# Kernel tuning notes

Hardware: AMD Instinct MI355X
Metric: run time of the kernel (lower is better)

The kernel has to match this reference:

```python
import jax, jax.numpy as jnp
import numpy as np

N_NODES = 10000
N_EDGES = 320000
IN_FEATS = 512
N_UNITS = 256
OUT_FEATS = 64
N_LAYERS = 6  # number of hidden GCNConv layers feeding the JK max


def setup_inputs() -> dict:
    key = jax.random.key(0)
    ks = jax.random.split(key, 8)
    h = jax.random.normal(ks[0], (N_NODES, IN_FEATS), dtype=jnp.float32)
    edge_index = jax.random.randint(ks[1], (2, N_EDGES), 0, N_NODES, dtype=jnp.int64)
    # learned parameters (glorot-ish scale)
    W0 = jax.random.normal(ks[2], (IN_FEATS, N_UNITS), dtype=jnp.float32) * (1.0 / np.sqrt(IN_FEATS))
    b0 = jnp.zeros((N_UNITS,), dtype=jnp.float32)
    Wh = jax.random.normal(ks[3], (N_LAYERS - 1, N_UNITS, N_UNITS), dtype=jnp.float32) * (1.0 / np.sqrt(N_UNITS))
    bh = jnp.zeros((N_LAYERS - 1, N_UNITS), dtype=jnp.float32)
    Wo = jax.random.normal(ks[4], (N_UNITS, OUT_FEATS), dtype=jnp.float32) * (1.0 / np.sqrt(N_UNITS))
    bo = jnp.zeros((OUT_FEATS,), dtype=jnp.float32)
    return {"h": h, "edge_index": edge_index, "W0": W0, "b0": b0,
            "Wh": Wh, "bh": bh, "Wo": Wo, "bo": bo}


def reference(h, edge_index, W0, b0, Wh, bh, Wo, bo):
    src = edge_index[0]
    dst = edge_index[1]
    n = h.shape[0]

    def conv_plain(x, W, b):
        # GCNConv with normalize=False: plain sum aggregation over edges, no self-loops
        m = x @ W                                   # [N, d]
        agg = jax.ops.segment_sum(m[src], dst, num_segments=n)
        return jax.nn.relu(agg + b)

    outs = []
    x = conv_plain(h, W0, b0)
    outs.append(x)
    for i in range(Wh.shape[0]):  # dropout is identity in eval mode
        x = conv_plain(x, Wh[i], bh[i])
        outs.append(x)

    # jumping-knowledge max aggregation over layer outputs
    x = jnp.max(jnp.stack(outs, axis=0), axis=0)    # [N, n_units]

    # final GCNConv with normalize=True (symmetric GCN norm, self-loops added)
    m = x @ Wo                                      # [N, out_feats]
    ones = jnp.ones(dst.shape, dtype=m.dtype)
    deg = jax.ops.segment_sum(ones, dst, num_segments=n) + 1.0  # +1 self loop
    dinv = deg ** -0.5
    coef = dinv[src] * dinv[dst]                    # [E]
    agg = jax.ops.segment_sum(m[src] * coef[:, None], dst, num_segments=n)
    agg = agg + m / deg[:, None] + bo               # self-loop term 1/deg_i
    return jax.nn.log_softmax(agg, axis=-1)
```

## Files before the change

### kernel.cpp

```cpp
#include <hip/hip_runtime.h>
#include <math.h>

#define N_NODES 10000
#define N_EDGES 320000
#define IN_FEATS 512
#define N_UNITS 256
#define OUT_FEATS 64
#define N_HID 5

typedef __attribute__((ext_vector_type(8))) short bf16x8;
typedef __attribute__((ext_vector_type(4))) float f32x4;

__device__ __forceinline__ unsigned short f2bf(float f) {
    union { float f; unsigned int u; } c; c.f = f;
    unsigned int u = c.u + 0x7FFFu + ((c.u >> 16) & 1u);
    return (unsigned short)(u >> 16);
}
__device__ __forceinline__ float bf2f(unsigned int b) {
    union { unsigned int u; float f; } c; c.u = (b & 0xffffu) << 16;
    return c.f;
}


__global__ void k_setup(const int* __restrict__ dst, int* __restrict__ deg,
                        const float* __restrict__ h, unsigned short* __restrict__ hb,
                        const float* __restrict__ W0, const float* __restrict__ Wh,
                        const float* __restrict__ Wo,
                        unsigned short* __restrict__ W0t, unsigned short* __restrict__ Wht,
                        unsigned short* __restrict__ Wot) {
    const int R1 = N_EDGES;
    const int R2 = N_NODES * IN_FEATS / 4;
    const int S0 = IN_FEATS * N_UNITS;
    const int SH = N_HID * N_UNITS * N_UNITS;
    const int SO = N_UNITS * OUT_FEATS;
    int t = blockIdx.x * blockDim.x + threadIdx.x;
    if (t < R1) {
        atomicAdd(&deg[dst[t]], 1);
    } else if (t < R1 + R2) {
        int u = t - R1;
        float4 v = reinterpret_cast<const float4*>(h)[u];
        ushort4 o;
        o.x = f2bf(v.x); o.y = f2bf(v.y); o.z = f2bf(v.z); o.w = f2bf(v.w);
        reinterpret_cast<ushort4*>(hb)[u] = o;
    } else {
        int u = t - R1 - R2;
        if (u < S0) {
            int k = u >> 8, n = u & 255;
            W0t[(size_t)n * IN_FEATS + k] = f2bf(W0[u]);
        } else if (u < S0 + SH) {
            int w = u - S0;
            int l = w >> 16, r = w & 65535;
            int k = r >> 8, n = r & 255;
            Wht[(size_t)l * 65536 + (size_t)n * N_UNITS + k] = f2bf(Wh[w]);
        } else if (u < S0 + SH + SO) {
            int w = u - S0 - SH;
            int k = w >> 6, n = w & 63;
            Wot[(size_t)n * N_UNITS + k] = f2bf(Wo[w]);
        }
    }
}


__global__ __launch_bounds__(1024) void k_scan(const int* __restrict__ deg,
                                               int* __restrict__ row_ptr,
                                               int* __restrict__ cursor,
                                               float* __restrict__ dinv,
                                               float* __restrict__ invdeg) {
    __shared__ int wsum[16];
    const int PER = 10;
    int t = threadIdx.x;
    int lane = t & 63, wid = t >> 6;
    int base = t * PER;

    int v[PER];
    int s = 0;
#pragma unroll
    for (int j = 0; j < PER; ++j) {
        int i = base + j;
        int d = (i < N_NODES) ? deg[i] : 0;
        v[j] = s;
        s += d;
    }
    int inc = s;
#pragma unroll
    for (int off = 1; off < 64; off <<= 1) {
        int y = __shfl_up(inc, off);
        if (lane >= off) inc += y;
    }
    if (lane == 63) wsum[wid] = inc;
    __syncthreads();
    if (wid == 0) {
        int w = (lane < 16) ? wsum[lane] : 0;
#pragma unroll
        for (int off = 1; off < 16; off <<= 1) {
            int y = __shfl_up(w, off);
            if (lane >= off) w += y;
        }
        if (lane < 16) wsum[lane] = w;
    }
    __syncthreads();
    int wave_excl = (wid == 0) ? 0 : wsum[wid - 1];
    int thread_excl = wave_excl + (inc - s);

#pragma unroll
    for (int j = 0; j < PER; ++j) {
        int i = base + j;
        if (i < N_NODES) {
            int rp = thread_excl + v[j];
            row_ptr[i] = rp;
            cursor[i]  = rp;
            int d = ((j + 1 < PER) ? v[j + 1] : s) - v[j];
            float dd = (float)(d + 1);
            dinv[i]   = rsqrtf(dd);
            invdeg[i] = 1.0f / dd;
        }
    }
    if (t == 1023) row_ptr[N_NODES] = thread_excl + s;
}

__global__ void k_fill(const int* __restrict__ src, const int* __restrict__ dst,
                       int* __restrict__ cursor, int* __restrict__ csr_src) {
    int e = blockIdx.x * blockDim.x + threadIdx.x;
    if (e < N_EDGES) {
        int p = atomicAdd(&cursor[dst[e]], 1);
        csr_src[p] = src[e];
    }
}


__global__ __launch_bounds__(256) void k_mgemm(const unsigned short* __restrict__ A,
                                               const unsigned short* __restrict__ Bt,
                                               unsigned short* __restrict__ C,
                                               const int M, const int K, const int Nld) {
    constexpr int BM = 64, BN = 64, BK = 32;
    __shared__ unsigned short As[2][BM * BK];
    __shared__ unsigned short Bs[2][BN * BK];

    const int tid  = threadIdx.x;
    const int wid  = tid >> 6;
    const int lane = tid & 63;
    const int wr   = wid >> 1;
    const int wc   = wid & 1;
    const int brow = blockIdx.y * BM;
    const int bcol = blockIdx.x * BN;

    const int lr = lane & 15;
    const int lk = lane >> 4;

    const int row  = tid >> 2;
    const int slot = tid & 3;
    const int sslot = slot ^ ((row >> 1) & 3);

    int gra = brow + row; if (gra >= M) gra = M - 1;
    const unsigned short* gpa = A + (size_t)gra * K + sslot * 8;
    const unsigned short* gpb = Bt + (size_t)(bcol + row) * K + sslot * 8;

    f32x4 acc[2][2];
#pragma unroll
    for (int m = 0; m < 2; ++m)
#pragma unroll
        for (int n = 0; n < 2; ++n)
            acc[m][n] = (f32x4){0.f, 0.f, 0.f, 0.f};

#define STAGE(buf, k0)                                                                      \
    do {                                                                                    \
        __builtin_amdgcn_global_load_lds(                                                   \
            (const __attribute__((address_space(1))) void*)(gpa + (k0)),                    \
            (__attribute__((address_space(3))) void*)(&As[(buf)][tid * 8]), 16, 0, 0);      \
        __builtin_amdgcn_global_load_lds(                                                   \
            (const __attribute__((address_space(1))) void*)(gpb + (k0)),                    \
            (__attribute__((address_space(3))) void*)(&Bs[(buf)][tid * 8]), 16, 0, 0);      \
    } while (0)

    STAGE(0, 0);
    __syncthreads();

    const int nk = K / BK;
    for (int kt = 0; kt < nk; ++kt) {
        const int cur = kt & 1;
        if (kt + 1 < nk) STAGE(cur ^ 1, (kt + 1) * BK);

        bf16x8 af[2], bfr[2];
#pragma unroll
        for (int m = 0; m < 2; ++m) {
            int ra = wr * 32 + m * 16 + lr;
            af[m] = *reinterpret_cast<const bf16x8*>(&As[cur][ra * BK + (lk ^ ((ra >> 1) & 3)) * 8]);
        }
#pragma unroll
        for (int n = 0; n < 2; ++n) {
            int rb = wc * 32 + n * 16 + lr;
            bfr[n] = *reinterpret_cast<const bf16x8*>(&Bs[cur][rb * BK + (lk ^ ((rb >> 1) & 3)) * 8]);
        }
#pragma unroll
        for (int m = 0; m < 2; ++m)
#pragma unroll
            for (int n = 0; n < 2; ++n)
                acc[m][n] = __builtin_amdgcn_mfma_f32_16x16x32_bf16(af[m], bfr[n], acc[m][n], 0, 0, 0);
        __syncthreads();
    }
#undef STAGE

#pragma unroll
    for (int m = 0; m < 2; ++m) {
#pragma unroll
        for (int r = 0; r < 4; ++r) {
            int orow = brow + wr * 32 + m * 16 + lk * 4 + r;
            if (orow < M) {
#pragma unroll
                for (int n = 0; n < 2; ++n) {
                    int ocol = bcol + wc * 32 + n * 16 + lr;
                    C[(size_t)orow * Nld + ocol] = f2bf(acc[m][n][r]);
                }
            }
        }
    }
}


__global__ __launch_bounds__(256) void k_wgemm(const unsigned short* __restrict__ A,
                                               const unsigned short* __restrict__ Bt,
                                               unsigned short* __restrict__ C,
                                               const int M, const int Nld) {
    constexpr int K = 256;
    __shared__ unsigned short As[64 * K];
    __shared__ unsigned short Bs[64 * K];

    const int tid  = threadIdx.x;
    const int wid  = tid >> 6;
    const int lane = tid & 63;
    const int lr   = lane & 15;
    const int lk   = lane >> 4;
    const int brow = blockIdx.y * 64;
    const int bcol = blockIdx.x * 64;

#pragma unroll
    for (int p = 0; p < 8; ++p) {
        int i = p * 256 + tid;
        int row = i >> 5, s = i & 31;
        int gr = brow + row; if (gr >= M) gr = M - 1;
        const unsigned short* gp = A + (size_t)gr * K + ((s ^ (row & 7)) * 8);
        __builtin_amdgcn_global_load_lds(
            (const __attribute__((address_space(1))) void*)gp,
            (__attribute__((address_space(3))) void*)(As + i * 8), 16, 0, 0);
    }
#pragma unroll
    for (int p = 0; p < 8; ++p) {
        int i = p * 256 + tid;
        int row = i >> 5, s = i & 31;
        const unsigned short* gp = Bt + (size_t)(bcol + row) * K + ((s ^ (row & 7)) * 8);
        __builtin_amdgcn_global_load_lds(
            (const __attribute__((address_space(1))) void*)gp,
            (__attribute__((address_space(3))) void*)(Bs + i * 8), 16, 0, 0);
    }
    __syncthreads();

    f32x4 acc[4];
#pragma unroll
    for (int n = 0; n < 4; ++n) acc[n] = (f32x4){0.f, 0.f, 0.f, 0.f};

    const int ra = (wid << 4) + lr;
    const unsigned short* Arow = As + ra * K;
    const int e = lr & 7;
#pragma unroll
    for (int kk = 0; kk < 8; ++kk) {
        bf16x8 av = *reinterpret_cast<const bf16x8*>(&Arow[(((kk << 2) + lk) ^ e) * 8]);
#pragma unroll
        for (int n = 0; n < 4; ++n) {
            const unsigned short* Brow = Bs + ((n << 4) + lr) * K;
            bf16x8 bv = *reinterpret_cast<const bf16x8*>(&Brow[(((kk << 2) + lk) ^ e) * 8]);
            acc[n] = __builtin_amdgcn_mfma_f32_16x16x32_bf16(av, bv, acc[n], 0, 0, 0);
        }
    }

#pragma unroll
    for (int n = 0; n < 4; ++n) {
#pragma unroll
        for (int r = 0; r < 4; ++r) {
            int orow = brow + (wid << 4) + (lk << 2) + r;
            if (orow < M) {
                int ocol = bcol + (n << 4) + lr;
                C[(size_t)orow * Nld + ocol] = f2bf(acc[n][r]);
            }
        }
    }
}


__global__ __launch_bounds__(256) void k_agg(const unsigned short* __restrict__ m,
                                             const int* __restrict__ row_ptr,
                                             const int* __restrict__ csr_src,
                                             const float* __restrict__ bias,
                                             unsigned short* __restrict__ x_out,
                                             unsigned short* __restrict__ jk,
                                             int init_jk) {
    int half = threadIdx.x >> 5;
    int lane = threadIdx.x & 31;
    int n = blockIdx.x * 8 + half;
    int s = row_ptr[n], e = row_ptr[n + 1];
    const uint4* mv = (const uint4*)m;

    float a[8];
#pragma unroll
    for (int j = 0; j < 8; ++j) a[j] = 0.f;

#define ACC8(u)                                        \
    do {                                               \
        a[0] += bf2f((u).x); a[1] += bf2f((u).x >> 16);\
        a[2] += bf2f((u).y); a[3] += bf2f((u).y >> 16);\
        a[4] += bf2f((u).z); a[5] += bf2f((u).z >> 16);\
        a[6] += bf2f((u).w); a[7] += bf2f((u).w >> 16);\
    } while (0)

    int i = s;
    for (; i + 7 < e; i += 8) {
        int idx[8];
#pragma unroll
        for (int q = 0; q < 8; ++q) idx[q] = csr_src[i + q];
        uint4 u[8];
#pragma unroll
        for (int q = 0; q < 8; ++q) u[q] = mv[(size_t)idx[q] * 32 + lane];
#pragma unroll
        for (int q = 0; q < 8; ++q) ACC8(u[q]);
    }
    for (; i < e; ++i) {
        uint4 u = mv[(size_t)csr_src[i] * 32 + lane];
        ACC8(u);
    }
#undef ACC8

    float4 b0 = ((const float4*)bias)[lane * 2];
    float4 b1 = ((const float4*)bias)[lane * 2 + 1];
    unsigned int hh[8];
    hh[0] = f2bf(fmaxf(a[0] + b0.x, 0.f));
    hh[1] = f2bf(fmaxf(a[1] + b0.y, 0.f));
    hh[2] = f2bf(fmaxf(a[2] + b0.z, 0.f));
    hh[3] = f2bf(fmaxf(a[3] + b0.w, 0.f));
    hh[4] = f2bf(fmaxf(a[4] + b1.x, 0.f));
    hh[5] = f2bf(fmaxf(a[5] + b1.y, 0.f));
    hh[6] = f2bf(fmaxf(a[6] + b1.z, 0.f));
    hh[7] = f2bf(fmaxf(a[7] + b1.w, 0.f));
    uint4 o;
    o.x = hh[0] | (hh[1] << 16);
    o.y = hh[2] | (hh[3] << 16);
    o.z = hh[4] | (hh[5] << 16);
    o.w = hh[6] | (hh[7] << 16);

    size_t idx = (size_t)n * 32 + lane;
    ((uint4*)x_out)[idx] = o;
    if (init_jk) {
        ((uint4*)jk)[idx] = o;
    } else {
        uint4 j = ((const uint4*)jk)[idx];
        auto mx2 = [](unsigned int nw, unsigned int od) {
            unsigned int lo_n = nw & 0xffffu, lo_o = od & 0xffffu;
            unsigned int hi_n = nw >> 16,     hi_o = od >> 16;
            unsigned int lo = lo_n > lo_o ? lo_n : lo_o;
            unsigned int hi = hi_n > hi_o ? hi_n : hi_o;
            return lo | (hi << 16);
        };
        uint4 w;
        w.x = mx2(o.x, j.x); w.y = mx2(o.y, j.y);
        w.z = mx2(o.z, j.z); w.w = mx2(o.w, j.w);
        ((uint4*)jk)[idx] = w;
    }
}


__global__ __launch_bounds__(256) void k_final(const unsigned short* __restrict__ mf,
                                               const int* __restrict__ row_ptr,
                                               const int* __restrict__ csr_src,
                                               const float* __restrict__ dinv,
                                               const float* __restrict__ invdeg,
                                               const float* __restrict__ bo,
                                               float* __restrict__ out) {
    int halfw = threadIdx.x >> 5;
    int wl = threadIdx.x & 31;
    const unsigned int* mfu = (const unsigned int*)mf;
    int n = blockIdx.x * 8 + halfw;
    int s = row_ptr[n], e = row_ptr[n + 1];

    float a0 = 0.f, a1 = 0.f;
    int i = s;
    for (; i + 3 < e; i += 4) {
        int i0 = csr_src[i], i1 = csr_src[i + 1], i2 = csr_src[i + 2], i3 = csr_src[i + 3];
        unsigned int u0 = mfu[(size_t)i0 * 32 + wl];
        unsigned int u1 = mfu[(size_t)i1 * 32 + wl];
        unsigned int u2 = mfu[(size_t)i2 * 32 + wl];
        unsigned int u3 = mfu[(size_t)i3 * 32 + wl];
        float d0 = dinv[i0], d1 = dinv[i1], d2 = dinv[i2], d3 = dinv[i3];
        a0 += bf2f(u0) * d0 + bf2f(u1) * d1 + bf2f(u2) * d2 + bf2f(u3) * d3;
        a1 += bf2f(u0 >> 16) * d0 + bf2f(u1 >> 16) * d1 + bf2f(u2 >> 16) * d2 + bf2f(u3 >> 16) * d3;
    }
    for (; i < e; ++i) {
        int sr = csr_src[i];
        unsigned int u = mfu[(size_t)sr * 32 + wl];
        float dv = dinv[sr];
        a0 += bf2f(u) * dv;
        a1 += bf2f(u >> 16) * dv;
    }
    float dn = dinv[n];
    a0 *= dn; a1 *= dn;
    unsigned int un = mfu[(size_t)n * 32 + wl];
    float idg = invdeg[n];
    float2 bo2 = ((const float2*)bo)[wl];
    a0 += bf2f(un) * idg + bo2.x;
    a1 += bf2f(un >> 16) * idg + bo2.y;

    float mx = fmaxf(a0, a1);
#pragma unroll
    for (int off = 16; off; off >>= 1) mx = fmaxf(mx, __shfl_xor(mx, off));
    float e0 = __expf(a0 - mx), e1 = __expf(a1 - mx);
    float sum = e0 + e1;
#pragma unroll
    for (int off = 16; off; off >>= 1) sum += __shfl_xor(sum, off);
    float ls = __logf(sum);
    float2 r;
    r.x = a0 - mx - ls;
    r.y = a1 - mx - ls;
    ((float2*)out)[(size_t)n * 32 + wl] = r;
}


extern "C" void kernel_launch(void* const* d_in, const int* in_sizes, int n_in,
                              void* d_out, int out_size, void* d_ws, size_t ws_size,
                              hipStream_t stream) {
    const float* h  = (const float*)d_in[0];
    const int*   ei = (const int*)d_in[1];
    const float* W0 = (const float*)d_in[2];
    const float* b0 = (const float*)d_in[3];
    const float* Wh = (const float*)d_in[4];
    const float* bh = (const float*)d_in[5];
    const float* Wo = (const float*)d_in[6];
    const float* bo = (const float*)d_in[7];

    const int* src = ei;
    const int* dst = ei + N_EDGES;

    char* p = (char*)d_ws;
    auto carve = [&](size_t bytes) {
        char* r = p;
        p += (bytes + 255) & ~(size_t)255;
        return r;
    };
    int*   deg     = (int*)  carve(N_NODES * 4);
    int*   row_ptr = (int*)  carve((N_NODES + 1) * 4);
    int*   cursor  = (int*)  carve(N_NODES * 4);
    int*   csr_src = (int*)  carve(N_EDGES * 4);
    float* dinv    = (float*)carve(N_NODES * 4);
    float* invdeg  = (float*)carve(N_NODES * 4);
    unsigned short* hb  = (unsigned short*)carve((size_t)N_NODES * IN_FEATS * 2);
    unsigned short* W0t = (unsigned short*)carve((size_t)IN_FEATS * N_UNITS * 2);
    unsigned short* Wht = (unsigned short*)carve((size_t)N_HID * N_UNITS * N_UNITS * 2);
    unsigned short* Wot = (unsigned short*)carve((size_t)N_UNITS * OUT_FEATS * 2);
    unsigned short* m   = (unsigned short*)carve((size_t)N_NODES * N_UNITS * 2);
    unsigned short* x   = (unsigned short*)carve((size_t)N_NODES * N_UNITS * 2);
    unsigned short* jk  = (unsigned short*)carve((size_t)N_NODES * N_UNITS * 2);
    unsigned short* mf  = (unsigned short*)carve((size_t)N_NODES * OUT_FEATS * 2);

    hipMemsetAsync(deg, 0, N_NODES * 4, stream);
    {
        const int total = N_EDGES + N_NODES * IN_FEATS / 4 +
                          IN_FEATS * N_UNITS + N_HID * N_UNITS * N_UNITS + N_UNITS * OUT_FEATS;
        k_setup<<<(total + 255) / 256, 256, 0, stream>>>(dst, deg, h, hb, W0, Wh, Wo,
                                                         W0t, Wht, Wot);
    }
    k_scan<<<1, 1024, 0, stream>>>(deg, row_ptr, cursor, dinv, invdeg);
    k_fill<<<(N_EDGES + 255) / 256, 256, 0, stream>>>(src, dst, cursor, csr_src);

    const int GBM = (N_NODES + 63) / 64;

    {
        dim3 g(N_UNITS / 64, GBM);
        k_mgemm<<<g, 256, 0, stream>>>(hb, W0t, m, N_NODES, IN_FEATS, N_UNITS);
    }
    k_agg<<<N_NODES / 8, 256, 0, stream>>>(m, row_ptr, csr_src, b0, x, jk, 1);

    for (int l = 0; l < N_HID; ++l) {
        dim3 g(N_UNITS / 64, GBM);
        k_wgemm<<<g, 256, 0, stream>>>(x, Wht + (size_t)l * N_UNITS * N_UNITS, m,
                                       N_NODES, N_UNITS);
        k_agg<<<N_NODES / 8, 256, 0, stream>>>(m, row_ptr, csr_src, bh + (size_t)l * N_UNITS,
                                               x, jk, 0);
    }

    {
        dim3 g(1, GBM);
        k_wgemm<<<g, 256, 0, stream>>>(jk, Wot, mf, N_NODES, OUT_FEATS);
    }
    k_final<<<N_NODES / 8, 256, 0, stream>>>(mf, row_ptr, csr_src, dinv, invdeg,
                                             bo, (float*)d_out);
}
```

Before: 253.3 us.

## Fuse fp32-to-bf16 input conversion into first GEMM and skip final x write

Removes the separate pass that converts the fp32 input features to bf16 in the setup kernel. The first-layer GEMM now loads fp32 rows directly, converts them in registers and stores bf16 into shared memory, using a full-width 256-column tile so each A row is read once. The last hidden aggregation layer also skips writing x, since only the JK max buffer is used afterwards. The trade-off is that the A loads become synchronous register loads instead of async global-to-LDS copies, and the larger tile means fewer blocks and more accumulator registers.

After: 256.6 us. About the same (+1.3%).

```diff
diff --git a/kernel.cpp b/kernel.cpp
--- a/kernel.cpp
+++ b/kernel.cpp
@@ -23,27 +23,19 @@
 
 
 __global__ void k_setup(const int* __restrict__ dst, int* __restrict__ deg,
-                        const float* __restrict__ h, unsigned short* __restrict__ hb,
                         const float* __restrict__ W0, const float* __restrict__ Wh,
                         const float* __restrict__ Wo,
                         unsigned short* __restrict__ W0t, unsigned short* __restrict__ Wht,
                         unsigned short* __restrict__ Wot) {
     const int R1 = N_EDGES;
-    const int R2 = N_NODES * IN_FEATS / 4;
     const int S0 = IN_FEATS * N_UNITS;
     const int SH = N_HID * N_UNITS * N_UNITS;
     const int SO = N_UNITS * OUT_FEATS;
     int t = blockIdx.x * blockDim.x + threadIdx.x;
     if (t < R1) {
         atomicAdd(&deg[dst[t]], 1);
-    } else if (t < R1 + R2) {
+    } else {
         int u = t - R1;
-        float4 v = reinterpret_cast<const float4*>(h)[u];
-        ushort4 o;
-        o.x = f2bf(v.x); o.y = f2bf(v.y); o.z = f2bf(v.z); o.w = f2bf(v.w);
-        reinterpret_cast<ushort4*>(hb)[u] = o;
-    } else {
-        int u = t - R1 - R2;
         if (u < S0) {
             int k = u >> 8, n = u & 255;
             W0t[(size_t)n * IN_FEATS + k] = f2bf(W0[u]);
@@ -128,88 +120,107 @@
 }
 
 
-__global__ __launch_bounds__(256) void k_mgemm(const unsigned short* __restrict__ A,
-                                               const unsigned short* __restrict__ Bt,
-                                               unsigned short* __restrict__ C,
-                                               const int M, const int K, const int Nld) {
-    constexpr int BM = 64, BN = 64, BK = 32;
-    __shared__ unsigned short As[2][BM * BK];
-    __shared__ unsigned short Bs[2][BN * BK];
+__global__ __launch_bounds__(256) void k_mgemm_h(const float* __restrict__ h,
+                                                 const unsigned short* __restrict__ Bt,
+                                                 unsigned short* __restrict__ C) {
+    constexpr int K = IN_FEATS;
+    constexpr int BM = 64, BN = 256, BK = 32;
+    __shared__ unsigned short As[2 * BM * BK];
+    __shared__ unsigned short Bs[2 * BN * BK];
 
     const int tid  = threadIdx.x;
     const int wid  = tid >> 6;
     const int lane = tid & 63;
     const int wr   = wid >> 1;
     const int wc   = wid & 1;
-    const int brow = blockIdx.y * BM;
-    const int bcol = blockIdx.x * BN;
+    const int brow = blockIdx.x * BM;
 
     const int lr = lane & 15;
     const int lk = lane >> 4;
 
-    const int row  = tid >> 2;
-    const int slot = tid & 3;
-    const int sslot = slot ^ ((row >> 1) & 3);
-
-    int gra = brow + row; if (gra >= M) gra = M - 1;
-    const unsigned short* gpa = A + (size_t)gra * K + sslot * 8;
-    const unsigned short* gpb = Bt + (size_t)(bcol + row) * K + sslot * 8;
-
-    f32x4 acc[2][2];
+    const int arow = tid >> 2;
+    const int aseg = tid & 3;
+    const int asl  = aseg ^ ((arow >> 1) & 3);
+    int gra = brow + arow; if (gra >= N_NODES) gra = N_NODES - 1;
+    const float* ap = h + (size_t)gra * K + aseg * 8;
+
+    f32x4 acc[2][8];
 #pragma unroll
     for (int m = 0; m < 2; ++m)
 #pragma unroll
-        for (int n = 0; n < 2; ++n)
+        for (int n = 0; n < 8; ++n)
             acc[m][n] = (f32x4){0.f, 0.f, 0.f, 0.f};
 
-#define STAGE(buf, k0)                                                                      \
-    do {                                                                                    \
-        __builtin_amdgcn_global_load_lds(                                                   \
-            (const __attribute__((address_space(1))) void*)(gpa + (k0)),                    \
-            (__attribute__((address_space(3))) void*)(&As[(buf)][tid * 8]), 16, 0, 0);      \
-        __builtin_amdgcn_global_load_lds(                                                   \
-            (const __attribute__((address_space(1))) void*)(gpb + (k0)),                    \
-            (__attribute__((address_space(3))) void*)(&Bs[(buf)][tid * 8]), 16, 0, 0);      \
+#define STAGE_A(buf, k0)                                                        \
+    do {                                                                        \
+        float4 v0 = *reinterpret_cast<const float4*>(ap + (k0));                \
+        float4 v1 = *reinterpret_cast<const float4*>(ap + (k0) + 4);            \
+        uint4 o;                                                                \
+        o.x = f2bf(v0.x) | ((unsigned)f2bf(v0.y) << 16);                        \
+        o.y = f2bf(v0.z) | ((unsigned)f2bf(v0.w) << 16);                        \
+        o.z = f2bf(v1.x) | ((unsigned)f2bf(v1.y) << 16);                        \
+        o.w = f2bf(v1.z) | ((unsigned)f2bf(v1.w) << 16);                        \
+        ((uint4*)As)[(buf) * 256 + arow * 4 + asl] = o;                         \
     } while (0)
 
-    STAGE(0, 0);
+#define STAGE_B(buf, k0)                                                                     \
+    do {                                                                                     \
+        _Pragma("unroll")                                                                    \
+        for (int p = 0; p < 4; ++p) {                                                        \
+            int i2 = p * 256 + tid;                                                          \
+            int row = i2 >> 2, sx = i2 & 3;                                                  \
+            const unsigned short* gp =                                                       \
+                Bt + (size_t)row * K + (k0) + ((sx ^ ((row >> 1) & 3)) * 8);                 \
+            __builtin_amdgcn_global_load_lds(                                                \
+                (const __attribute__((address_space(1))) void*)gp,                           \
+                (__attribute__((address_space(3))) void*)(Bs + (buf) * BN * BK + i2 * 8),    \
+                16, 0, 0);                                                                   \
+        }                                                                                    \
+    } while (0)
+
+    STAGE_A(0, 0);
+    STAGE_B(0, 0);
     __syncthreads();
 
     const int nk = K / BK;
     for (int kt = 0; kt < nk; ++kt) {
         const int cur = kt & 1;
-        if (kt + 1 < nk) STAGE(cur ^ 1, (kt + 1) * BK);
-
-        bf16x8 af[2], bfr[2];
+        if (kt + 1 < nk) {
+            STAGE_A(cur ^ 1, (kt + 1) * BK);
+            STAGE_B(cur ^ 1, (kt + 1) * BK);
+        }
+
+        bf16x8 af[2], bfr[8];
 #pragma unroll
         for (int m = 0; m < 2; ++m) {
             int ra = wr * 32 + m * 16 + lr;
-            af[m] = *reinterpret_cast<const bf16x8*>(&As[cur][ra * BK + (lk ^ ((ra >> 1) & 3)) * 8]);
-        }
-#pragma unroll
-        for (int n = 0; n < 2; ++n) {
-            int rb = wc * 32 + n * 16 + lr;
-            bfr[n] = *reinterpret_cast<const bf16x8*>(&Bs[cur][rb * BK + (lk ^ ((rb >> 1) & 3)) * 8]);
+            af[m] = *reinterpret_cast<const bf16x8*>(&As[cur * BM * BK + ra * BK + (lk ^ ((ra >> 1) & 3)) * 8]);
+        }
+#pragma unroll
+        for (int n = 0; n < 8; ++n) {
+            int rb = wc * 128 + n * 16 + lr;
+            bfr[n] = *reinterpret_cast<const bf16x8*>(&Bs[cur * BN * BK + rb * BK + (lk ^ ((rb >> 1) & 3)) * 8]);
         }
 #pragma unroll
         for (int m = 0; m < 2; ++m)
 #pragma unroll
-            for (int n = 0; n < 2; ++n)
+            for (int n = 0; n < 8; ++n)
                 acc[m][n] = __builtin_amdgcn_mfma_f32_16x16x32_bf16(af[m], bfr[n], acc[m][n], 0, 0, 0);
         __syncthreads();
     }
-#undef STAGE
+#undef STAGE_A
+#undef STAGE_B
 
 #pragma unroll
     for (int m = 0; m < 2; ++m) {
 #pragma unroll
         for (int r = 0; r < 4; ++r) {
             int orow = brow + wr * 32 + m * 16 + lk * 4 + r;
-            if (orow < M) {
-#pragma unroll
-                for (int n = 0; n < 2; ++n) {
-                    int ocol = bcol + wc * 32 + n * 16 + lr;
-                    C[(size_t)orow * Nld + ocol] = f2bf(acc[m][n][r]);
+            if (orow < N_NODES) {
+#pragma unroll
+                for (int n = 0; n < 8; ++n) {
+                    int ocol = wc * 128 + n * 16 + lr;
+                    C[(size_t)orow * N_UNITS + ocol] = f2bf(acc[m][n][r]);
                 }
             }
         }
@@ -292,7 +303,7 @@
                                              const float* __restrict__ bias,
                                              unsigned short* __restrict__ x_out,
                                              unsigned short* __restrict__ jk,
-                                             int init_jk) {
+                                             int init_jk, int write_x) {
     int half = threadIdx.x >> 5;
     int lane = threadIdx.x & 31;
     int n = blockIdx.x * 8 + half;
@@ -346,7 +357,7 @@
     o.w = hh[6] | (hh[7] << 16);
 
     size_t idx = (size_t)n * 32 + lane;
-    ((uint4*)x_out)[idx] = o;
+    if (write_x) ((uint4*)x_out)[idx] = o;
     if (init_jk) {
         ((uint4*)jk)[idx] = o;
     } else {
@@ -448,7 +459,6 @@
     int*   csr_src = (int*)  carve(N_EDGES * 4);
     float* dinv    = (float*)carve(N_NODES * 4);
     float* invdeg  = (float*)carve(N_NODES * 4);
-    unsigned short* hb  = (unsigned short*)carve((size_t)N_NODES * IN_FEATS * 2);
     unsigned short* W0t = (unsigned short*)carve((size_t)IN_FEATS * N_UNITS * 2);
     unsigned short* Wht = (unsigned short*)carve((size_t)N_HID * N_UNITS * N_UNITS * 2);
     unsigned short* Wot = (unsigned short*)carve((size_t)N_UNITS * OUT_FEATS * 2);
@@ -459,9 +469,9 @@
 
     hipMemsetAsync(deg, 0, N_NODES * 4, stream);
     {
-        const int total = N_EDGES + N_NODES * IN_FEATS / 4 +
+        const int total = N_EDGES +
                           IN_FEATS * N_UNITS + N_HID * N_UNITS * N_UNITS + N_UNITS * OUT_FEATS;
-        k_setup<<<(total + 255) / 256, 256, 0, stream>>>(dst, deg, h, hb, W0, Wh, Wo,
+        k_setup<<<(total + 255) / 256, 256, 0, stream>>>(dst, deg, W0, Wh, Wo,
                                                          W0t, Wht, Wot);
     }
     k_scan<<<1, 1024, 0, stream>>>(deg, row_ptr, cursor, dinv, invdeg);
@@ -469,18 +479,15 @@
 
     const int GBM = (N_NODES + 63) / 64;
 
-    {
-        dim3 g(N_UNITS / 64, GBM);
-        k_mgemm<<<g, 256, 0, stream>>>(hb, W0t, m, N_NODES, IN_FEATS, N_UNITS);
-    }
-    k_agg<<<N_NODES / 8, 256, 0, stream>>>(m, row_ptr, csr_src, b0, x, jk, 1);
+    k_mgemm_h<<<GBM, 256, 0, stream>>>(h, W0t, m);
+    k_agg<<<N_NODES / 8, 256, 0, stream>>>(m, row_ptr, csr_src, b0, x, jk, 1, 1);
 
     for (int l = 0; l < N_HID; ++l) {
         dim3 g(N_UNITS / 64, GBM);
         k_wgemm<<<g, 256, 0, stream>>>(x, Wht + (size_t)l * N_UNITS * N_UNITS, m,
                                        N_NODES, N_UNITS);
         k_agg<<<N_NODES / 8, 256, 0, stream>>>(m, row_ptr, csr_src, bh + (size_t)l * N_UNITS,
-                                               x, jk, 0);
+                                               x, jk, 0, (l < N_HID - 1) ? 1 : 0);
     }
 
     {
```
